# Kernel tuning notes

Hardware: AMD Instinct MI355X
Metric: run time of the kernel (lower is better)

The kernel has to match this reference:

```python
import jax, jax.numpy as jnp
import numpy as np

N_NODES = 50000
N_EDGES = 800000
D = 256


def gcn_conv(x, edge_index, W, b, n_nodes):
    """PyG-style GCNConv: add self-loops, symmetric norm, linear, scatter-add."""
    # add self loops
    loops = jnp.arange(n_nodes, dtype=edge_index.dtype)
    src = jnp.concatenate([edge_index[0], loops])  # message sources
    dst = jnp.concatenate([edge_index[1], loops])  # aggregation targets
    # symmetric normalization: deg computed on targets (incl. self loops)
    deg = jax.ops.segment_sum(jnp.ones_like(dst, dtype=x.dtype), dst,
                              num_segments=n_nodes)
    dinv = jnp.where(deg > 0, jax.lax.rsqrt(deg), 0.0)
    norm = dinv[src] * dinv[dst]  # [E+N]
    h = x @ W  # [N, out]
    msg = h[src] * norm[:, None]  # gather + scale, [E+N, out]
    out = jax.ops.segment_sum(msg, dst, num_segments=n_nodes)  # scatter-add
    return out + b


def setup_inputs() -> dict:
    key = jax.random.key(0)
    k1, k2, k3, k4 = jax.random.split(key, 4)
    x = jax.random.normal(k1, (N_NODES, D), dtype=jnp.float32)
    edge_index = jax.random.randint(k2, (2, N_EDGES), 0, N_NODES, dtype=jnp.int64)
    s = 1.0 / np.sqrt(D)
    W1 = jax.random.normal(k3, (D, D), dtype=jnp.float32) * s
    W2 = jax.random.normal(k4, (D, D), dtype=jnp.float32) * s
    b1 = jnp.zeros((D,), dtype=jnp.float32)
    b2 = jnp.zeros((D,), dtype=jnp.float32)
    return {"x": x, "edge_index": edge_index, "W1": W1, "b1": b1,
            "W2": W2, "b2": b2}


def reference(x, edge_index, W1, b1, W2, b2):
    n = x.shape[0]
    out = gcn_conv(x, edge_index, W1, b1, n)
    out = jax.nn.relu(out)  # dropout is identity in eval mode (p=0.2 in train)
    out = out + gcn_conv(x, edge_index, W2, b2, n)
    return out
```

## Files before the change

kernel.cpp:

```cpp
#include <hip/hip_runtime.h>
#include <hip/hip_bf16.h>

#define DIM 256
#define CAP 64
#define GEMM_G 128

typedef short bf16x8 __attribute__((ext_vector_type(8)));
typedef float f32x4  __attribute__((ext_vector_type(4)));
typedef float f32x4v __attribute__((ext_vector_type(4)));
typedef unsigned short u16x4 __attribute__((ext_vector_type(4)));

__device__ __forceinline__ unsigned short f2b(float f) {
    union { __hip_bfloat16 h; unsigned short u; } cv;
    cv.h = __float2bfloat16(f);
    return cv.u;
}
__device__ __forceinline__ float b2f(unsigned short u) {
    return __uint_as_float(((unsigned)u) << 16);
}

#define OFF_FILL   0
#define OFF_WT1    262144
#define OFF_WT2    393216
#define OFF_BUCKET 524288
#define OFF_AGG    6924544ull
#define OFF_YB     32524544ull
#define NEED_BF    (OFF_YB + 25600000ull)

__global__ void k_fill(const int* __restrict__ src, const int* __restrict__ dst,
                       int* __restrict__ fill, unsigned short* __restrict__ bucket, int nE) {
    int e = blockIdx.x * blockDim.x + threadIdx.x;
    if (e < nE) {
        int d = dst[e];
        int pos = atomicAdd(&fill[d], 1);
        if (pos < CAP) bucket[d * CAP + pos] = (unsigned short)src[e];
    }
}

__global__ void k_wt(const float* __restrict__ W1, const float* __restrict__ W2,
                     unsigned short* __restrict__ wt1, unsigned short* __restrict__ wt2) {
    int t = blockIdx.x * blockDim.x + threadIdx.x;
    if (t < DIM * DIM) {
        int k = t & 255, nn = t >> 8;
        wt1[t] = f2b(W1[k * DIM + nn]);
        wt2[t] = f2b(W2[k * DIM + nn]);
    }
}

__global__ void k_yb(const float* __restrict__ x, const int* __restrict__ fill,
                     ushort4* __restrict__ yb, int n4) {
    int t = blockIdx.x * blockDim.x + threadIdx.x;
    if (t < n4) {
        float d = rsqrtf((float)(1 + fill[t >> 6]));
        f32x4v v = __builtin_nontemporal_load((const f32x4v*)x + t);
        ushort4 r;
        r.x = f2b(d * v.x); r.y = f2b(d * v.y);
        r.z = f2b(d * v.z); r.w = f2b(d * v.w);
        yb[t] = r;
    }
}

__global__ void k_agg_bf(const ushort4* __restrict__ yb, const int* __restrict__ fill,
                         const unsigned short* __restrict__ bucket,
                         ushort4* __restrict__ aggbf, int n) {
    int node = (blockIdx.x * blockDim.x + threadIdx.x) >> 6;
    int lane = threadIdx.x & 63;
    if (node >= n) return;

    ushort4 s = yb[(size_t)node * 64 + lane];
    float a0 = b2f(s.x), a1 = b2f(s.y), a2 = b2f(s.z), a3 = b2f(s.w);

    int c = fill[node];
    float di = rsqrtf((float)(1 + c));
    if (c > CAP) c = CAP;
    const unsigned short* bk = bucket + (size_t)node * CAP;

    int k = 0;
    for (; k + 4 <= c; k += 4) {
        u16x4 j4 = __builtin_nontemporal_load((const u16x4*)(bk + k));
        ushort4 r0 = yb[(size_t)j4.x * 64 + lane];
        ushort4 r1 = yb[(size_t)j4.y * 64 + lane];
        ushort4 r2 = yb[(size_t)j4.z * 64 + lane];
        ushort4 r3 = yb[(size_t)j4.w * 64 + lane];
        a0 += b2f(r0.x) + b2f(r1.x) + b2f(r2.x) + b2f(r3.x);
        a1 += b2f(r0.y) + b2f(r1.y) + b2f(r2.y) + b2f(r3.y);
        a2 += b2f(r0.z) + b2f(r1.z) + b2f(r2.z) + b2f(r3.z);
        a3 += b2f(r0.w) + b2f(r1.w) + b2f(r2.w) + b2f(r3.w);
    }
    for (; k < c; k++) {
        int j = bk[k];
        ushort4 r = yb[(size_t)j * 64 + lane];
        a0 += b2f(r.x); a1 += b2f(r.y); a2 += b2f(r.z); a3 += b2f(r.w);
    }

    ushort4 r;
    r.x = f2b(a0 * di); r.y = f2b(a1 * di);
    r.z = f2b(a2 * di); r.w = f2b(a3 * di);
    unsigned long long rbits;
    __builtin_memcpy(&rbits, &r, 8);
    __builtin_nontemporal_store(rbits,
        (unsigned long long*)&aggbf[(size_t)node * 64 + lane]);
}

__global__ void k_agg_f32(const float4* __restrict__ x4, const int* __restrict__ fill,
                          const unsigned short* __restrict__ bucket,
                          ushort4* __restrict__ aggbf, int n) {
    int node = (blockIdx.x * blockDim.x + threadIdx.x) >> 6;
    int lane = threadIdx.x & 63;
    if (node >= n) return;

    int c = fill[node];
    float di = rsqrtf((float)(1 + c));
    if (c > CAP) c = CAP;

    float4 xi = x4[(size_t)node * 64 + lane];
    float a0 = di * xi.x, a1 = di * xi.y, a2 = di * xi.z, a3 = di * xi.w;

    const unsigned short* bk = bucket + (size_t)node * CAP;
    for (int k = 0; k < c; k++) {
        int j = bk[k];
        float dj = rsqrtf((float)(1 + fill[j]));
        float4 xj = x4[(size_t)j * 64 + lane];
        a0 += dj * xj.x; a1 += dj * xj.y; a2 += dj * xj.z; a3 += dj * xj.w;
    }
    ushort4 r;
    r.x = f2b(a0 * di); r.y = f2b(a1 * di);
    r.z = f2b(a2 * di); r.w = f2b(a3 * di);
    aggbf[(size_t)node * 64 + lane] = r;
}

__launch_bounds__(256, 4)
__global__ void k_gemm(const short* __restrict__ aggbf,
                       const short* __restrict__ wt1, const short* __restrict__ wt2,
                       const float* __restrict__ b1, const float* __restrict__ b2,
                       float* __restrict__ out, int n, int ntiles) {
    __shared__ uint4 bs[4096];

    int c0  = blockIdx.y * 64;
    int tid = threadIdx.x;

#pragma unroll
    for (int i = 0; i < 16; i++) {
        int l = tid + i * 256;
        int m = l >> 11, rem = l & 2047, nn = rem >> 5, p = rem & 31;
        const short* base = (m == 0) ? wt1 : wt2;
        const uint4* sp = (const uint4*)(base + ((size_t)(c0 + nn)) * DIM) + p;
        bs[(m << 11) + (nn << 5) + (p ^ (nn & 31))] = *sp;
    }
    __syncthreads();

    int lane = tid & 63;
    int wave = tid >> 6;
    int lrow = lane & 15;
    int quad = lane >> 4;

    float bb1[4], bb2[4];
#pragma unroll
    for (int ct = 0; ct < 4; ct++) {
        bb1[ct] = b1[c0 + ct * 16 + lrow];
        bb2[ct] = b2[c0 + ct * 16 + lrow];
    }

    for (int t = blockIdx.x; t < ntiles; t += gridDim.x) {
        int rowbase = t * 128 + wave * 32;
        int r0 = rowbase + lrow;       if (r0 >= n) r0 = 0;
        int r1 = rowbase + 16 + lrow;  if (r1 >= n) r1 = 0;
        const short* ap0 = aggbf + (size_t)r0 * DIM + quad * 8;
        const short* ap1 = aggbf + (size_t)r1 * DIM + quad * 8;

        f32x4 acc1[2][4], acc2[2][4];
#pragma unroll
        for (int sub = 0; sub < 2; sub++)
#pragma unroll
            for (int ct = 0; ct < 4; ct++) {
                acc1[sub][ct] = (f32x4){0.f, 0.f, 0.f, 0.f};
                acc2[sub][ct] = (f32x4){0.f, 0.f, 0.f, 0.f};
            }

        bf16x8 a0 = *(const bf16x8*)(ap0);
        bf16x8 a1 = *(const bf16x8*)(ap1);
#pragma unroll
        for (int s = 0; s < 8; s++) {
            bf16x8 na0 = a0, na1 = a1;
            if (s < 7) {
                na0 = *(const bf16x8*)(ap0 + (s + 1) * 32);
                na1 = *(const bf16x8*)(ap1 + (s + 1) * 32);
            }
#pragma unroll
            for (int ct = 0; ct < 4; ct++) {
                int nn = ct * 16 + lrow;
                int ch = (4 * s + quad) ^ (nn & 31);
                uint4 u1 = bs[(nn << 5) + ch];
                uint4 u2 = bs[2048 + (nn << 5) + ch];
                bf16x8 w1f, w2f;
                __builtin_memcpy(&w1f, &u1, 16);
                __builtin_memcpy(&w2f, &u2, 16);
                acc1[0][ct] = __builtin_amdgcn_mfma_f32_16x16x32_bf16(a0, w1f, acc1[0][ct], 0, 0, 0);
                acc1[1][ct] = __builtin_amdgcn_mfma_f32_16x16x32_bf16(a1, w1f, acc1[1][ct], 0, 0, 0);
                acc2[0][ct] = __builtin_amdgcn_mfma_f32_16x16x32_bf16(a0, w2f, acc2[0][ct], 0, 0, 0);
                acc2[1][ct] = __builtin_amdgcn_mfma_f32_16x16x32_bf16(a1, w2f, acc2[1][ct], 0, 0, 0);
            }
            a0 = na0; a1 = na1;
        }

#pragma unroll
        for (int sub = 0; sub < 2; sub++) {
            int rb = rowbase + sub * 16 + quad * 4;
#pragma unroll
            for (int ct = 0; ct < 4; ct++) {
                int col = c0 + ct * 16 + lrow;
#pragma unroll
                for (int i = 0; i < 4; i++) {
                    int row = rb + i;
                    if (row < n) {
                        float v = fmaxf(acc1[sub][ct][i] + bb1[ct], 0.f)
                                + acc2[sub][ct][i] + bb2[ct];
                        __builtin_nontemporal_store(v, &out[(size_t)row * DIM + col]);
                    }
                }
            }
        }
    }
}

extern "C" void kernel_launch(void* const* d_in, const int* in_sizes, int n_in,
                              void* d_out, int out_size, void* d_ws, size_t ws_size,
                              hipStream_t stream) {
    const float* x  = (const float*)d_in[0];
    const int*   ei = (const int*)d_in[1];
    const float* W1 = (const float*)d_in[2];
    const float* b1 = (const float*)d_in[3];
    const float* W2 = (const float*)d_in[4];
    const float* b2 = (const float*)d_in[5];
    float* out = (float*)d_out;

    int n = in_sizes[0] / DIM;
    int E = in_sizes[1] / 2;
    const int* src = ei;
    const int* dst = ei + E;

    char* ws = (char*)d_ws;
    int*            fill   = (int*)(ws + OFF_FILL);
    unsigned short* wt1    = (unsigned short*)(ws + OFF_WT1);
    unsigned short* wt2    = (unsigned short*)(ws + OFF_WT2);
    unsigned short* bucket = (unsigned short*)(ws + OFF_BUCKET);
    ushort4*        aggbf  = (ushort4*)(ws + OFF_AGG);
    ushort4*        yb     = (ushort4*)(ws + OFF_YB);

    (void)hipMemsetAsync(fill, 0, n * sizeof(int), stream);

    k_fill<<<(E + 255) / 256, 256, 0, stream>>>(src, dst, fill, bucket, E);
    k_wt  <<<(DIM * DIM + 255) / 256, 256, 0, stream>>>(W1, W2, wt1, wt2);

    int aggBlocks = (n * 64 + 255) / 256;
    bool use_bf = (ws_size >= NEED_BF);
    if (use_bf) {
        int n4 = n * DIM / 4;
        k_yb<<<(n4 + 255) / 256, 256, 0, stream>>>(x, fill, yb, n4);
        k_agg_bf<<<aggBlocks, 256, 0, stream>>>(yb, fill, bucket, aggbf, n);
    } else {
        k_agg_f32<<<aggBlocks, 256, 0, stream>>>((const float4*)x, fill, bucket, aggbf, n);
    }

    int ntiles = (n + 127) / 128;
    dim3 ggrid(GEMM_G, DIM / 64);
    k_gemm<<<ggrid, 256, 0, stream>>>((const short*)aggbf, (const short*)wt1,
                                      (const short*)wt2, b1, b2, out, n, ntiles);
}
```

Before: 270.1 us.

## Fuse prep kernels, widen aggregation to 16B loads, enlarge GEMM blocks

Merges the weight transpose and the scaled bf16 conversion of x into a single prep launch, so one kernel launch goes away. The gather-aggregation now handles two nodes per wavefront, with each lane loading 8 bf16 values as a uint4 instead of 4. This halves the number of load instructions per edge. The GEMM moves to 512-thread blocks covering 256-row tiles, which halves the shared-memory weight staging per row processed, at the cost of fewer blocks and possible register pressure.

```diff
diff --git a/kernel.cpp b/kernel.cpp
--- a/kernel.cpp
+++ b/kernel.cpp
@@ -3,11 +3,10 @@
 
 #define DIM 256
 #define CAP 64
-#define GEMM_G 128
+#define GEMM_BX 128
 
 typedef short bf16x8 __attribute__((ext_vector_type(8)));
 typedef float f32x4  __attribute__((ext_vector_type(4)));
-typedef float f32x4v __attribute__((ext_vector_type(4)));
 typedef unsigned short u16x4 __attribute__((ext_vector_type(4)));
 
 __device__ __forceinline__ unsigned short f2b(float f) {
@@ -17,6 +16,12 @@
 }
 __device__ __forceinline__ float b2f(unsigned short u) {
     return __uint_as_float(((unsigned)u) << 16);
+}
+__device__ __forceinline__ void acc8(uint4 u, float* a) {
+    a[0] += __uint_as_float(u.x << 16); a[1] += __uint_as_float(u.x & 0xffff0000u);
+    a[2] += __uint_as_float(u.y << 16); a[3] += __uint_as_float(u.y & 0xffff0000u);
+    a[4] += __uint_as_float(u.z << 16); a[5] += __uint_as_float(u.z & 0xffff0000u);
+    a[6] += __uint_as_float(u.w << 16); a[7] += __uint_as_float(u.w & 0xffff0000u);
 }
 
 #define OFF_FILL   0
@@ -37,38 +42,49 @@
     }
 }
 
-__global__ void k_wt(const float* __restrict__ W1, const float* __restrict__ W2,
-                     unsigned short* __restrict__ wt1, unsigned short* __restrict__ wt2) {
-    int t = blockIdx.x * blockDim.x + threadIdx.x;
-    if (t < DIM * DIM) {
-        int k = t & 255, nn = t >> 8;
-        wt1[t] = f2b(W1[k * DIM + nn]);
-        wt2[t] = f2b(W2[k * DIM + nn]);
-    }
-}
-
-__global__ void k_yb(const float* __restrict__ x, const int* __restrict__ fill,
-                     ushort4* __restrict__ yb, int n4) {
-    int t = blockIdx.x * blockDim.x + threadIdx.x;
-    if (t < n4) {
-        float d = rsqrtf((float)(1 + fill[t >> 6]));
-        f32x4v v = __builtin_nontemporal_load((const f32x4v*)x + t);
-        ushort4 r;
-        r.x = f2b(d * v.x); r.y = f2b(d * v.y);
-        r.z = f2b(d * v.z); r.w = f2b(d * v.w);
-        yb[t] = r;
-    }
-}
-
-__global__ void k_agg_bf(const ushort4* __restrict__ yb, const int* __restrict__ fill,
+__global__ void k_prep(const float* __restrict__ x, const int* __restrict__ fill,
+                       uint4* __restrict__ yb,
+                       const float* __restrict__ W1, const float* __restrict__ W2,
+                       unsigned short* __restrict__ wt1, unsigned short* __restrict__ wt2,
+                       int nybBlocks, int n8) {
+    if ((int)blockIdx.x < nybBlocks) {
+        int t = blockIdx.x * 256 + threadIdx.x;
+        if (t < n8) {
+            float d = rsqrtf((float)(1 + fill[t >> 5]));
+            const f32x4* xp = (const f32x4*)x + t * 2;
+            f32x4 v0 = xp[0], v1 = xp[1];
+            uint4 r;
+            r.x = (unsigned)f2b(d * v0.x) | ((unsigned)f2b(d * v0.y) << 16);
+            r.y = (unsigned)f2b(d * v0.z) | ((unsigned)f2b(d * v0.w) << 16);
+            r.z = (unsigned)f2b(d * v1.x) | ((unsigned)f2b(d * v1.y) << 16);
+            r.w = (unsigned)f2b(d * v1.z) | ((unsigned)f2b(d * v1.w) << 16);
+            yb[t] = r;
+        }
+    } else {
+        int t = (blockIdx.x - nybBlocks) * 256 + threadIdx.x;
+        if (t < DIM * DIM) {
+            int k = t & 255, nn = t >> 8;
+            wt1[t] = f2b(W1[k * DIM + nn]);
+            wt2[t] = f2b(W2[k * DIM + nn]);
+        }
+    }
+}
+
+__global__ void k_agg_bf(const uint4* __restrict__ yb, const int* __restrict__ fill,
                          const unsigned short* __restrict__ bucket,
-                         ushort4* __restrict__ aggbf, int n) {
-    int node = (blockIdx.x * blockDim.x + threadIdx.x) >> 6;
+                         uint4* __restrict__ aggbf, int n) {
+    int t    = blockIdx.x * blockDim.x + threadIdx.x;
+    int wid  = t >> 6;
     int lane = threadIdx.x & 63;
+    int node = wid * 2 + (lane >> 5);
+    int h    = lane & 31;
     if (node >= n) return;
 
-    ushort4 s = yb[(size_t)node * 64 + lane];
-    float a0 = b2f(s.x), a1 = b2f(s.y), a2 = b2f(s.z), a3 = b2f(s.w);
+    float a[8];
+    uint4 s = yb[(size_t)node * 32 + h];
+#pragma unroll
+    for (int i = 0; i < 8; i++) a[i] = 0.f;
+    acc8(s, a);
 
     int c = fill[node];
     float di = rsqrtf((float)(1 + c));
@@ -77,29 +93,28 @@
 
     int k = 0;
     for (; k + 4 <= c; k += 4) {
-        u16x4 j4 = __builtin_nontemporal_load((const u16x4*)(bk + k));
-        ushort4 r0 = yb[(size_t)j4.x * 64 + lane];
-        ushort4 r1 = yb[(size_t)j4.y * 64 + lane];
-        ushort4 r2 = yb[(size_t)j4.z * 64 + lane];
-        ushort4 r3 = yb[(size_t)j4.w * 64 + lane];
-        a0 += b2f(r0.x) + b2f(r1.x) + b2f(r2.x) + b2f(r3.x);
-        a1 += b2f(r0.y) + b2f(r1.y) + b2f(r2.y) + b2f(r3.y);
-        a2 += b2f(r0.z) + b2f(r1.z) + b2f(r2.z) + b2f(r3.z);
-        a3 += b2f(r0.w) + b2f(r1.w) + b2f(r2.w) + b2f(r3.w);
+        u16x4 j4 = *(const u16x4*)(bk + k);
+        uint4 r0 = yb[(size_t)j4.x * 32 + h];
+        uint4 r1 = yb[(size_t)j4.y * 32 + h];
+        uint4 r2 = yb[(size_t)j4.z * 32 + h];
+        uint4 r3 = yb[(size_t)j4.w * 32 + h];
+        acc8(r0, a); acc8(r1, a); acc8(r2, a); acc8(r3, a);
     }
     for (; k < c; k++) {
-        int j = bk[k];
-        ushort4 r = yb[(size_t)j * 64 + lane];
-        a0 += b2f(r.x); a1 += b2f(r.y); a2 += b2f(r.z); a3 += b2f(r.w);
-    }
-
-    ushort4 r;
-    r.x = f2b(a0 * di); r.y = f2b(a1 * di);
-    r.z = f2b(a2 * di); r.w = f2b(a3 * di);
-    unsigned long long rbits;
-    __builtin_memcpy(&rbits, &r, 8);
-    __builtin_nontemporal_store(rbits,
-        (unsigned long long*)&aggbf[(size_t)node * 64 + lane]);
+        uint4 r = yb[(size_t)bk[k] * 32 + h];
+        acc8(r, a);
+    }
+
+    uint4 r;
+    r.x = (unsigned)f2b(a[0] * di) | ((unsigned)f2b(a[1] * di) << 16);
+    r.y = (unsigned)f2b(a[2] * di) | ((unsigned)f2b(a[3] * di) << 16);
+    r.z = (unsigned)f2b(a[4] * di) | ((unsigned)f2b(a[5] * di) << 16);
+    r.w = (unsigned)f2b(a[6] * di) | ((unsigned)f2b(a[7] * di) << 16);
+    uint4* dstp = &aggbf[(size_t)node * 32 + h];
+    __builtin_nontemporal_store(r.x, &((unsigned*)dstp)[0]);
+    __builtin_nontemporal_store(r.y, &((unsigned*)dstp)[1]);
+    __builtin_nontemporal_store(r.z, &((unsigned*)dstp)[2]);
+    __builtin_nontemporal_store(r.w, &((unsigned*)dstp)[3]);
 }
 
 __global__ void k_agg_f32(const float4* __restrict__ x4, const int* __restrict__ fill,
@@ -129,7 +144,7 @@
     aggbf[(size_t)node * 64 + lane] = r;
 }
 
-__launch_bounds__(256, 4)
+__launch_bounds__(512, 4)
 __global__ void k_gemm(const short* __restrict__ aggbf,
                        const short* __restrict__ wt1, const short* __restrict__ wt2,
                        const float* __restrict__ b1, const float* __restrict__ b2,
@@ -140,8 +155,8 @@
     int tid = threadIdx.x;
 
 #pragma unroll
-    for (int i = 0; i < 16; i++) {
-        int l = tid + i * 256;
+    for (int i = 0; i < 8; i++) {
+        int l = tid + i * 512;
         int m = l >> 11, rem = l & 2047, nn = rem >> 5, p = rem & 31;
         const short* base = (m == 0) ? wt1 : wt2;
         const uint4* sp = (const uint4*)(base + ((size_t)(c0 + nn)) * DIM) + p;
@@ -162,7 +177,7 @@
     }
 
     for (int t = blockIdx.x; t < ntiles; t += gridDim.x) {
-        int rowbase = t * 128 + wave * 32;
+        int rowbase = t * 256 + wave * 32;
         int r0 = rowbase + lrow;       if (r0 >= n) r0 = 0;
         int r1 = rowbase + 16 + lrow;  if (r1 >= n) r1 = 0;
         const short* ap0 = aggbf + (size_t)r0 * DIM + quad * 8;
@@ -244,26 +259,30 @@
     unsigned short* wt1    = (unsigned short*)(ws + OFF_WT1);
     unsigned short* wt2    = (unsigned short*)(ws + OFF_WT2);
     unsigned short* bucket = (unsigned short*)(ws + OFF_BUCKET);
-    ushort4*        aggbf  = (ushort4*)(ws + OFF_AGG);
-    ushort4*        yb     = (ushort4*)(ws + OFF_YB);
+    char*           aggp   = ws + OFF_AGG;
+    uint4*          yb     = (uint4*)(ws + OFF_YB);
 
     (void)hipMemsetAsync(fill, 0, n * sizeof(int), stream);
 
     k_fill<<<(E + 255) / 256, 256, 0, stream>>>(src, dst, fill, bucket, E);
-    k_wt  <<<(DIM * DIM + 255) / 256, 256, 0, stream>>>(W1, W2, wt1, wt2);
-
-    int aggBlocks = (n * 64 + 255) / 256;
+
     bool use_bf = (ws_size >= NEED_BF);
     if (use_bf) {
-        int n4 = n * DIM / 4;
-        k_yb<<<(n4 + 255) / 256, 256, 0, stream>>>(x, fill, yb, n4);
-        k_agg_bf<<<aggBlocks, 256, 0, stream>>>(yb, fill, bucket, aggbf, n);
+        int n8 = n * (DIM / 8);
+        int nybBlocks = (n8 + 255) / 256;
+        k_prep<<<nybBlocks + 256, 256, 0, stream>>>(x, fill, yb, W1, W2, wt1, wt2,
+                                                    nybBlocks, n8);
+        int aggBlocks = ((n + 1) / 2 * 64 + 255) / 256;
+        k_agg_bf<<<aggBlocks, 256, 0, stream>>>(yb, fill, bucket, (uint4*)aggp, n);
     } else {
-        k_agg_f32<<<aggBlocks, 256, 0, stream>>>((const float4*)x, fill, bucket, aggbf, n);
-    }
-
-    int ntiles = (n + 127) / 128;
-    dim3 ggrid(GEMM_G, DIM / 64);
-    k_gemm<<<ggrid, 256, 0, stream>>>((const short*)aggbf, (const short*)wt1,
+        k_prep<<<256, 256, 0, stream>>>(x, fill, yb, W1, W2, wt1, wt2, 0, 0);
+        int aggBlocks = (n * 64 + 255) / 256;
+        k_agg_f32<<<aggBlocks, 256, 0, stream>>>((const float4*)x, fill, bucket,
+                                                 (ushort4*)aggp, n);
+    }
+
+    int ntiles = (n + 255) / 256;
+    dim3 ggrid(GEMM_BX, DIM / 64);
+    k_gemm<<<ggrid, 512, 0, stream>>>((const short*)aggp, (const short*)wt1,
                                       (const short*)wt2, b1, b2, out, n, ntiles);
 }
```

Result: slower. 419.4 us (+55.3%).
